# Kernel tuning notes

Measured on AMD Instinct MI355X. Metric: run time of the kernel, lower is better.

Reference implementation:

```python
import jax, jax.numpy as jnp
import numpy as np

GROUPS = 32
EPS = 1e-5


def group_norm(x, gamma, beta):
    # x: [B, C, H, W]; normalize over (C//G, H, W) within each of G groups
    B, C, H, W = x.shape
    xg = x.reshape(B, GROUPS, C // GROUPS, H, W)
    mean = xg.mean(axis=(2, 3, 4), keepdims=True)
    var = xg.var(axis=(2, 3, 4), keepdims=True)
    xg = (xg - mean) * jax.lax.rsqrt(var + EPS)
    x = xg.reshape(B, C, H, W)
    return x * gamma[None, :, None, None] + beta[None, :, None, None]


def conv1x1(x, W, b):
    # 1x1 conv == pointwise linear over channels. x: [B,C,H,W], W: [Cout,Cin]
    return jnp.einsum('oc,bchw->bohw', W, x) + b[None, :, None, None]


def setup_inputs() -> dict:
    key = jax.random.key(0)
    ks = jax.random.split(key, 6)
    B, C, H, W = 16, 512, 32, 32
    scale = 1.0 / np.sqrt(C)  # ~kaiming-ish init for 1x1 convs
    return {
        'x': jax.random.normal(ks[0], (B, C, H, W), jnp.float32),
        'gn_gamma': jnp.ones((C,), jnp.float32),
        'gn_beta': jnp.zeros((C,), jnp.float32),
        'Wq': jax.random.normal(ks[1], (C, C), jnp.float32) * scale,
        'bq': jnp.zeros((C,), jnp.float32),
        'Wk': jax.random.normal(ks[2], (C, C), jnp.float32) * scale,
        'bk': jnp.zeros((C,), jnp.float32),
        'Wv': jax.random.normal(ks[3], (C, C), jnp.float32) * scale,
        'bv': jnp.zeros((C,), jnp.float32),
        'Wp': jax.random.normal(ks[4], (C, C), jnp.float32) * scale,
        'bp': jnp.zeros((C,), jnp.float32),
    }


def reference(x, gn_gamma, gn_beta, Wq, bq, Wk, bk, Wv, bv, Wp, bp):
    B, C, H, W = x.shape
    h = group_norm(x, gn_gamma, gn_beta)
    q = conv1x1(h, Wq, bq).reshape(B, C, H * W)  # [B,C,T]
    k = conv1x1(h, Wk, bk).reshape(B, C, H * W)
    v = conv1x1(h, Wv, bv).reshape(B, C, H * W)
    # scores [B, T(query), S(key)] = q^T k, scaled by C^{-1/2}
    w = jnp.einsum('bct,bcs->bts', q, k) * (C ** -0.5)
    w = jax.nn.softmax(w, axis=-1)
    h = jnp.einsum('bts,bcs->bct', w, v).reshape(B, C, H, W)
    h = conv1x1(h, Wp, bp)
    return x + h
```

## Files before the change

kernel.cpp:

```cpp
#include <hip/hip_runtime.h>

typedef unsigned short u16;
typedef __bf16 bf16x8 __attribute__((ext_vector_type(8)));
typedef float f32x4 __attribute__((ext_vector_type(4)));
typedef float f32x16 __attribute__((ext_vector_type(16)));

__device__ __forceinline__ u16 f2bf(float f) {
    unsigned u = __builtin_bit_cast(unsigned, f);
    u += 0x7fffu + ((u >> 16) & 1u);
    return (u16)(u >> 16);
}
__device__ __forceinline__ float bf2f(u16 h) {
    return __builtin_bit_cast(float, (unsigned)h << 16);
}

#define GLDS16(g, l) __builtin_amdgcn_global_load_lds( \
    (const __attribute__((address_space(1))) void*)(g), \
    (__attribute__((address_space(3))) void*)(l), 16, 0, 0)

#define QK_SCALE 0.044194173824159216f

__global__ __launch_bounds__(256) void convert_kernel(
    const float* __restrict__ Wq, const float* __restrict__ Wk,
    const float* __restrict__ Wv, const float* __restrict__ Wp,
    const float* __restrict__ bq, const float* __restrict__ bk,
    const float* __restrict__ bv,
    u16* __restrict__ Wqkv, u16* __restrict__ Wpb, float* __restrict__ bqkv,
    float* __restrict__ rsum)
{
    int idx = blockIdx.x * 256 + threadIdx.x;
    if (idx < 786432) {
        int which = idx >> 18;
        int off   = idx & 262143;
        if (which == 0)
            Wqkv[idx] = f2bf(Wq[off] * QK_SCALE);
        else
            Wqkv[idx] = f2bf(((which == 1) ? Wk : Wv)[off]);
    } else {
        int off = idx - 786432;
        Wpb[off] = f2bf(Wp[off]);
    }
    if (idx < 1536) {
        float bvv = (idx < 512) ? bq[idx] * QK_SCALE
                  : (idx < 1024) ? bk[idx & 511] : bv[idx & 511];
        bqkv[idx] = bvv;
    }
    if (idx < 16384) rsum[idx] = 0.f;
}

__global__ __launch_bounds__(256) void gn_stats(
    const float* __restrict__ x, float2* __restrict__ stats)
{
    const int g = blockIdx.x, b = blockIdx.y, tid = threadIdx.x;
    const float* xg = x + ((size_t)b * 512 + (size_t)g * 16) * 1024;

    float s = 0.f, s2 = 0.f;
    const float4* x4 = (const float4*)xg;
    #pragma unroll 4
    for (int i = tid; i < 4096; i += 256) {
        float4 v = x4[i];
        s  += v.x + v.y + v.z + v.w;
        s2 += v.x * v.x + v.y * v.y + v.z * v.z + v.w * v.w;
    }
    #pragma unroll
    for (int off = 32; off; off >>= 1) {
        s  += __shfl_down(s, off);
        s2 += __shfl_down(s2, off);
    }
    __shared__ float rs[4], rs2[4];
    const int w = tid >> 6;
    if ((tid & 63) == 0) { rs[w] = s; rs2[w] = s2; }
    __syncthreads();
    if (tid == 0) {
        float S  = rs[0] + rs[1] + rs[2] + rs[3];
        float S2 = rs2[0] + rs2[1] + rs2[2] + rs2[3];
        float mean = S * (1.f / 16384.f);
        float var  = S2 * (1.f / 16384.f) - mean * mean;
        stats[b * 32 + g] = make_float2(mean, rsqrtf(var + 1e-5f));
    }
}

__global__ __launch_bounds__(256) void gn_apply(
    const float* __restrict__ x, const float* __restrict__ gamma,
    const float* __restrict__ beta, const float2* __restrict__ stats,
    u16* __restrict__ ht)
{
    const int tc = blockIdx.x, b = blockIdx.y, tid = threadIdx.x;
    const int t0 = tc * 32;

    __shared__ float2 st[32];
    __shared__ float ga[512], be[512];
    __shared__ __align__(16) u16 tile[512 * 32];

    if (tid < 32) st[tid] = stats[b * 32 + tid];
    for (int c = tid; c < 512; c += 256) { ga[c] = gamma[c]; be[c] = beta[c]; }
    __syncthreads();

    #pragma unroll
    for (int pass = 0; pass < 16; pass++) {
        const int c = pass * 32 + (tid >> 3);
        const int f = tid & 7;
        float4 v = *(const float4*)(x + ((size_t)(b * 512 + c)) * 1024 + t0 + f * 4);
        float2 s = st[c >> 4];
        float sc = s.y * ga[c];
        float sh = be[c] - s.x * sc;
        ushort4 hv = {f2bf(v.x * sc + sh), f2bf(v.y * sc + sh),
                      f2bf(v.z * sc + sh), f2bf(v.w * sc + sh)};
        const int slot = f ^ (c & 7) ^ ((c >> 3) & 7);
        *(ushort4*)(tile + c * 32 + slot * 4) = hv;
    }
    __syncthreads();

    #pragma unroll
    for (int p = 0; p < 8; p++) {
        const int t = p * 4 + (tid >> 6);
        const int l = tid & 63;
        u16 tmp[8];
        #pragma unroll
        for (int e = 0; e < 8; e++) {
            const int c = l * 8 + e;
            const int slot = (t >> 2) ^ (c & 7) ^ ((c >> 3) & 7);
            tmp[e] = tile[c * 32 + slot * 4 + (t & 3)];
        }
        *(uint4*)(ht + ((size_t)b * 1024 + t0 + t) * 512 + l * 8) = *(uint4*)tmp;
    }
}

template <int MODE>
__global__ __launch_bounds__(512, 2) void gemm_big(
    const u16* __restrict__ A, const u16* __restrict__ B,
    size_t strideA, size_t strideB, int lda, int ldb, int K,
    u16* __restrict__ o0, u16* __restrict__ o1, u16* __restrict__ o2,
    const float* __restrict__ bias)
{
    __shared__ __align__(16) u16 smem[73728];
    u16* As = smem;
    u16* Bs = smem + 49152;

    const int tid  = threadIdx.x;
    const int lane = tid & 63;
    const int wave = tid >> 6;
    const int wm   = (wave & 3) * 64;
    const int wn   = (wave >> 2) * 64;

    const int gx = gridDim.x, gy = gridDim.y;
    int f = blockIdx.x + gx * (blockIdx.y + gy * blockIdx.z);
    const int nwg = gx * gy * (int)gridDim.z;
    f = (f & 7) * (nwg >> 3) + (f >> 3);
    const int bx  = f % gx;
    const int byz = f / gx;
    const int by  = byz % gy;
    const int b   = byz / gy;

    const u16* Ab = A + (size_t)b * strideA + (size_t)by * 256 * lda;
    const u16* Bb = B + (size_t)b * strideB + (size_t)bx * 128 * ldb;

    const int srow = tid >> 3;
    const int sc   = tid & 7;
    const int scg  = sc ^ (srow & 7);

    const u16* aSrc[4]; int aDst[4];
    #pragma unroll
    for (int u = 0; u < 4; u++) {
        aSrc[u] = Ab + (size_t)(u * 64 + srow) * lda + scg * 8;
        aDst[u] = (u * 64 + srow) * 64 + sc * 8;
    }
    const u16* bSrc[2]; int bDst[2];
    #pragma unroll
    for (int u = 0; u < 2; u++) {
        bSrc[u] = Bb + (size_t)(u * 64 + srow) * ldb + scg * 8;
        bDst[u] = (u * 64 + srow) * 64 + sc * 8;
    }

    const int l15 = lane & 15, lh = lane >> 4, rx = lane & 7;
    int aOff[4][2], bOff[4][2];
    #pragma unroll
    for (int i = 0; i < 4; i++)
        #pragma unroll
        for (int ks = 0; ks < 2; ks++) {
            const int slot = ((ks << 2) + lh) ^ rx;
            aOff[i][ks] = (wm + i * 16 + l15) * 64 + slot * 8;
            bOff[i][ks] = (wn + i * 16 + l15) * 64 + slot * 8;
        }

    f32x4 acc[4][4] = {};
    const int NT = K >> 6;

    #pragma unroll
    for (int u = 0; u < 4; u++) GLDS16(aSrc[u], As + aDst[u]);
    #pragma unroll
    for (int u = 0; u < 2; u++) GLDS16(bSrc[u], Bs + bDst[u]);
    #pragma unroll
    for (int u = 0; u < 4; u++) GLDS16(aSrc[u] + 64, As + 16384 + aDst[u]);
    #pragma unroll
    for (int u = 0; u < 2; u++) GLDS16(bSrc[u] + 64, Bs + 8192 + bDst[u]);

    int cbuf = 0, sbuf = 2;
    for (int t = 0; t < NT; ++t) {
        if (t == NT - 1) asm volatile("s_waitcnt vmcnt(0)" ::: "memory");
        else             asm volatile("s_waitcnt vmcnt(6)" ::: "memory");
        __builtin_amdgcn_s_barrier();

        const u16* Ac = As + cbuf * 16384;
        const u16* Bc = Bs + cbuf * 8192;
        u16* Asb = As + sbuf * 16384;
        u16* Bsb = Bs + sbuf * 8192;
        const int ko = (t + 2) * 64;
        const bool pf = (t + 2 < NT);

        if (pf) {
            GLDS16(aSrc[0] + ko, Asb + aDst[0]);
            GLDS16(aSrc[1] + ko, Asb + aDst[1]);
            GLDS16(bSrc[0] + ko, Bsb + bDst[0]);
        }
        {
            bf16x8 af[4], bfr[4];
            #pragma unroll
            for (int i = 0; i < 4; i++) {
                af[i]  = *(const bf16x8*)(Ac + aOff[i][0]);
                bfr[i] = *(const bf16x8*)(Bc + bOff[i][0]);
            }
            __builtin_amdgcn_s_setprio(1);
            #pragma unroll
            for (int mi = 0; mi < 4; mi++)
                #pragma unroll
                for (int nj = 0; nj < 4; nj++)
                    acc[mi][nj] = __builtin_amdgcn_mfma_f32_16x16x32_bf16(
                        af[mi], bfr[nj], acc[mi][nj], 0, 0, 0);
            __builtin_amdgcn_s_setprio(0);
        }
        if (pf) {
            GLDS16(aSrc[2] + ko, Asb + aDst[2]);
            GLDS16(aSrc[3] + ko, Asb + aDst[3]);
            GLDS16(bSrc[1] + ko, Bsb + bDst[1]);
        }
        {
            bf16x8 af[4], bfr[4];
            #pragma unroll
            for (int i = 0; i < 4; i++) {
                af[i]  = *(const bf16x8*)(Ac + aOff[i][1]);
                bfr[i] = *(const bf16x8*)(Bc + bOff[i][1]);
            }
            __builtin_amdgcn_s_setprio(1);
            #pragma unroll
            for (int mi = 0; mi < 4; mi++)
                #pragma unroll
                for (int nj = 0; nj < 4; nj++)
                    acc[mi][nj] = __builtin_amdgcn_mfma_f32_16x16x32_bf16(
                        af[mi], bfr[nj], acc[mi][nj], 0, 0, 0);
            __builtin_amdgcn_s_setprio(0);
        }

        cbuf = (cbuf == 2) ? 0 : cbuf + 1;
        sbuf = (sbuf == 2) ? 0 : sbuf + 1;
    }

    const int N0 = bx * 128;
    const int M0 = by * 256;

    if (N0 < 1024) {
        u16* dst = (N0 < 512) ? o0 : o1;
        const int nn0 = N0 & 511;
        #pragma unroll
        for (int nj = 0; nj < 4; nj++) {
            const int n = wn + nj * 16 + l15;
            const float bv = bias[N0 + n];
            #pragma unroll
            for (int mi = 0; mi < 4; mi++) {
                const int mq = M0 + wm + mi * 16 + lh * 4;
                const size_t base = ((size_t)b * 1024 + mq) * 512 + nn0 + n;
                dst[base]        = f2bf(acc[mi][nj][0] + bv);
                dst[base + 512]  = f2bf(acc[mi][nj][1] + bv);
                dst[base + 1024] = f2bf(acc[mi][nj][2] + bv);
                dst[base + 1536] = f2bf(acc[mi][nj][3] + bv);
            }
        }
    } else {
        __syncthreads();
        #pragma unroll
        for (int mi = 0; mi < 4; mi++) {
            const int mq = wm + mi * 16 + lh * 4;
            #pragma unroll
            for (int nj = 0; nj < 4; nj++) {
                const int n = wn + nj * 16 + l15;
                const float bv = bias[N0 + n];
                ushort4 hv = {f2bf(acc[mi][nj][0] + bv), f2bf(acc[mi][nj][1] + bv),
                              f2bf(acc[mi][nj][2] + bv), f2bf(acc[mi][nj][3] + bv)};
                *(ushort4*)((char*)smem + n * 512 +
                            (((mq >> 3) ^ (n & 31)) << 4) + ((mq >> 2) & 1) * 8) = hv;
            }
        }
        __syncthreads();
        #pragma unroll
        for (int p = 0; p < 8; p++) {
            const int n  = p * 16 + (tid >> 5);
            const int gi = tid & 31;
            uint4 v4 = *(const uint4*)((char*)smem + n * 512 +
                                       ((gi ^ (n & 31)) << 4));
            u16* dst = o2 + ((size_t)b * 512 + (N0 - 1024) + n) * 1024 + M0;
            *(uint4*)(dst + gi * 8) = v4;
        }
    }
}

template <int MODE>
__global__ __launch_bounds__(256, 4) void gemm128(
    const u16* __restrict__ A, const u16* __restrict__ B,
    size_t strideA, size_t strideB, int lda, int ldb, int K,
    u16* __restrict__ o0,
    float* __restrict__ fo, const float* __restrict__ bias,
    const float* __restrict__ xres)
{
    __shared__ __align__(16) u16 sm[16384];
    u16* As = sm;
    u16* Bs = sm + 8192;

    const int tid   = threadIdx.x;
    const int lane  = tid & 63;
    const int wave  = tid >> 6;
    const int wm    = (wave >> 1) * 64;
    const int wn    = (wave & 1) * 64;
    const int l31   = lane & 31;
    const int khalf = lane >> 5;

    const int gx = gridDim.x, gy = gridDim.y;
    int f = blockIdx.x + gx * (blockIdx.y + gy * blockIdx.z);
    const int nwg = gx * gy * (int)gridDim.z;
    f = (f & 7) * (nwg >> 3) + (f >> 3);
    const int bx  = f % gx;
    const int byz = f / gx;
    const int by  = byz % gy;
    const int b   = byz / gy;

    const u16* Ab = A + (size_t)b * strideA + (size_t)by * 128 * lda;
    const u16* Bb = B + (size_t)b * strideB + (size_t)bx * 128 * ldb;

    const int srow = lane >> 3;
    const int sc   = lane & 7;
    const int scg  = sc ^ srow;

    f32x16 acc[2][2] = {};

    for (int k0 = 0; k0 < K; k0 += 64) {
        __syncthreads();
        #pragma unroll
        for (int s = 0; s < 4; s++) {
            const int r = wave * 32 + s * 8 + srow;
            GLDS16(Ab + (size_t)r * lda + k0 + scg * 8, As + r * 64 + sc * 8);
            GLDS16(Bb + (size_t)r * ldb + k0 + scg * 8, Bs + r * 64 + sc * 8);
        }
        __syncthreads();

        #pragma unroll
        for (int ks = 0; ks < 4; ks++) {
            const int cidx = ks * 2 + khalf;
            const int slot = (cidx ^ (lane & 7)) * 8;
            bf16x8 af[2], bfr[2];
            #pragma unroll
            for (int i = 0; i < 2; i++)
                af[i] = *(const bf16x8*)(As + (wm + i * 32 + l31) * 64 + slot);
            #pragma unroll
            for (int j = 0; j < 2; j++)
                bfr[j] = *(const bf16x8*)(Bs + (wn + j * 32 + l31) * 64 + slot);
            #pragma unroll
            for (int i = 0; i < 2; i++)
                #pragma unroll
                for (int j = 0; j < 2; j++)
                    acc[i][j] = __builtin_amdgcn_mfma_f32_32x32x16_bf16(
                        af[i], bfr[j], acc[i][j], 0, 0, 0);
        }
    }

    const int N0 = bx * 128;
    const int M0 = by * 128;

    if (MODE != 3) {
        __syncthreads();
        float rinv_[2];
        if (MODE == 2) {
            #pragma unroll
            for (int j = 0; j < 2; j++)
                rinv_[j] = 1.0f / xres[(size_t)b * 1024 + N0 + wn + j * 32 + l31];
        }
        #pragma unroll
        for (int i = 0; i < 2; i++) {
            #pragma unroll
            for (int j = 0; j < 2; j++) {
                const int n = wn + j * 32 + l31;
                #pragma unroll
                for (int g = 0; g < 4; g++) {
                    const int m = wm + 4 * khalf + i * 32 + 8 * g;
                    float a0 = acc[i][j][4 * g],     a1 = acc[i][j][4 * g + 1];
                    float a2 = acc[i][j][4 * g + 2], a3 = acc[i][j][4 * g + 3];
                    if (MODE == 1) {
                        a0 = __expf(a0); a1 = __expf(a1);
                        a2 = __expf(a2); a3 = __expf(a3);
                    }
                    if (MODE == 2) {
                        a0 *= rinv_[j]; a1 *= rinv_[j];
                        a2 *= rinv_[j]; a3 *= rinv_[j];
                    }
                    ushort4 hv = {f2bf(a0), f2bf(a1), f2bf(a2), f2bf(a3)};
                    *(ushort4*)(sm + n * 128 + (((m >> 3) ^ (n & 15)) << 3) + (m & 7)) = hv;
                }
            }
        }
        __syncthreads();
        #pragma unroll
        for (int p = 0; p < 8; p++) {
            const int n  = p * 16 + (tid >> 4);
            const int gi = tid & 15;
            uint4 v = *(const uint4*)(sm + n * 128 + ((gi ^ (n & 15)) << 3));
            u16* dst;
            if (MODE == 1) dst = o0 + ((size_t)b * 1024 + N0 + n) * 1024 + M0;
            else           dst = o0 + ((size_t)b * 1024 + N0 + n) * 512 + M0;
            *(uint4*)(dst + gi * 8) = v;
            if (MODE == 1) {
                unsigned wd_[4] = {v.x, v.y, v.z, v.w};
                float rsm = 0.f;
                #pragma unroll
                for (int q = 0; q < 4; q++)
                    rsm += __builtin_bit_cast(float, wd_[q] << 16)
                         + __builtin_bit_cast(float, wd_[q] & 0xffff0000u);
                #pragma unroll
                for (int off = 1; off < 16; off <<= 1)
                    rsm += __shfl_xor(rsm, off);
                if (gi == 0)
                    atomicAdd(fo + ((size_t)b * 1024 + N0 + n), rsm);
            }
        }
    } else {
        float* smf = (float*)sm;
        #pragma unroll
        for (int i = 0; i < 2; i++) {
            __syncthreads();
            #pragma unroll
            for (int j = 0; j < 2; j++) {
                const int n = wn + j * 32 + l31;
                #pragma unroll
                for (int g = 0; g < 4; g++) {
                    const int mIdx = 4 * khalf + 8 * g + ((wm >> 6) << 5);
                    float4 v4 = {acc[i][j][4 * g],     acc[i][j][4 * g + 1],
                                 acc[i][j][4 * g + 2], acc[i][j][4 * g + 3]};
                    *(float4*)(smf + n * 64 + (((mIdx >> 2) ^ (n & 15)) << 2)) = v4;
                }
            }
            __syncthreads();
            #pragma unroll
            for (int p = 0; p < 8; p++) {
                const int n  = p * 16 + (tid >> 4);
                const int gi = tid & 15;
                float4 v = *(const float4*)(smf + n * 64 + ((gi ^ (n & 15)) << 2));
                const int m = (gi & 7) * 4 + ((gi >> 3) << 6) + 32 * i;
                const size_t off = ((size_t)b * 512 + N0 + n) * 1024 + M0 + m;
                const float bv = bias[N0 + n];
                const float4 xv = *(const float4*)(xres + off);
                float4 ov = {v.x + bv + xv.x, v.y + bv + xv.y,
                             v.z + bv + xv.z, v.w + bv + xv.w};
                *(float4*)(fo + off) = ov;
            }
        }
    }
}

extern "C" void kernel_launch(void* const* d_in, const int* in_sizes, int n_in,
                              void* d_out, int out_size, void* d_ws, size_t ws_size,
                              hipStream_t stream)
{
    const float* x     = (const float*)d_in[0];
    const float* gamma = (const float*)d_in[1];
    const float* beta  = (const float*)d_in[2];
    const float* Wq    = (const float*)d_in[3];
    const float* bq    = (const float*)d_in[4];
    const float* Wk    = (const float*)d_in[5];
    const float* bk    = (const float*)d_in[6];
    const float* Wv    = (const float*)d_in[7];
    const float* bv    = (const float*)d_in[8];
    const float* Wp    = (const float*)d_in[9];
    const float* bp    = (const float*)d_in[10];

    char* ws = (char*)d_ws;
    u16*   Wqkv   = (u16*)(ws + 0);
    u16*   Wpb    = (u16*)(ws + 1572864);
    float* bqkv   = (float*)(ws + 2097152);
    u16*   ht     = (u16*)(ws + 2105344);
    u16*   kt     = (u16*)(ws + 18882560);
    u16*   vv     = (u16*)(ws + 35659776);
    u16*   scores = (u16*)(ws + 52436992);
    u16*   qt  = (u16*)d_out;
    float2* stats = (float2*)((char*)d_out + 16777216);
    float* rsum   = (float*)((char*)d_out + 16781312);
    u16*   h2  = ht;
    float* out = (float*)d_out;

    convert_kernel<<<4096, 256, 0, stream>>>(Wq, Wk, Wv, Wp, bq, bk, bv,
                                             Wqkv, Wpb, bqkv, rsum);
    gn_stats<<<dim3(32, 16), 256, 0, stream>>>(x, stats);
    gn_apply<<<dim3(32, 16), 256, 0, stream>>>(x, gamma, beta, stats, ht);

    gemm_big<0><<<dim3(12, 4, 16), 512, 0, stream>>>(
        ht, Wqkv, 524288, 0, 512, 512, 512,
        qt, kt, vv, bqkv);

    gemm128<1><<<dim3(8, 8, 16), 256, 0, stream>>>(
        kt, qt, 524288, 524288, 512, 512, 512,
        scores, rsum, nullptr, nullptr);

    gemm128<2><<<dim3(8, 4, 16), 256, 0, stream>>>(
        vv, scores, 524288, 1048576, 1024, 1024, 1024,
        h2, nullptr, nullptr, rsum);

    gemm128<3><<<dim3(4, 8, 16), 256, 0, stream>>>(
        h2, Wpb, 524288, 0, 512, 512, 512,
        nullptr, out, bp, x);
}
```

Before: 227.1 us.

## Switch gemm128 to 16x16x32 MFMA tiles and fuse weight conversion with GN stats

```diff
diff --git a/kernel.cpp b/kernel.cpp
--- a/kernel.cpp
+++ b/kernel.cpp
@@ -3,7 +3,6 @@
 typedef unsigned short u16;
 typedef __bf16 bf16x8 __attribute__((ext_vector_type(8)));
 typedef float f32x4 __attribute__((ext_vector_type(4)));
-typedef float f32x16 __attribute__((ext_vector_type(16)));
 
 __device__ __forceinline__ u16 f2bf(float f) {
     unsigned u = __builtin_bit_cast(unsigned, f);
@@ -20,38 +19,42 @@
 
 #define QK_SCALE 0.044194173824159216f
 
-__global__ __launch_bounds__(256) void convert_kernel(
+__global__ __launch_bounds__(256) void fused_pre(
     const float* __restrict__ Wq, const float* __restrict__ Wk,
     const float* __restrict__ Wv, const float* __restrict__ Wp,
     const float* __restrict__ bq, const float* __restrict__ bk,
     const float* __restrict__ bv,
     u16* __restrict__ Wqkv, u16* __restrict__ Wpb, float* __restrict__ bqkv,
-    float* __restrict__ rsum)
-{
-    int idx = blockIdx.x * 256 + threadIdx.x;
-    if (idx < 786432) {
-        int which = idx >> 18;
-        int off   = idx & 262143;
-        if (which == 0)
-            Wqkv[idx] = f2bf(Wq[off] * QK_SCALE);
-        else
-            Wqkv[idx] = f2bf(((which == 1) ? Wk : Wv)[off]);
-    } else {
-        int off = idx - 786432;
-        Wpb[off] = f2bf(Wp[off]);
-    }
-    if (idx < 1536) {
-        float bvv = (idx < 512) ? bq[idx] * QK_SCALE
-                  : (idx < 1024) ? bk[idx & 511] : bv[idx & 511];
-        bqkv[idx] = bvv;
-    }
-    if (idx < 16384) rsum[idx] = 0.f;
-}
-
-__global__ __launch_bounds__(256) void gn_stats(
+    float* __restrict__ rsum,
     const float* __restrict__ x, float2* __restrict__ stats)
 {
-    const int g = blockIdx.x, b = blockIdx.y, tid = threadIdx.x;
+    __shared__ float rs[4], rs2[4];
+    const int tid = threadIdx.x;
+
+    if (blockIdx.x < 4096) {
+        int idx = blockIdx.x * 256 + tid;
+        if (idx < 786432) {
+            int which = idx >> 18;
+            int off   = idx & 262143;
+            if (which == 0)
+                Wqkv[idx] = f2bf(Wq[off] * QK_SCALE);
+            else
+                Wqkv[idx] = f2bf(((which == 1) ? Wk : Wv)[off]);
+        } else {
+            int off = idx - 786432;
+            Wpb[off] = f2bf(Wp[off]);
+        }
+        if (idx < 1536) {
+            float bvv = (idx < 512) ? bq[idx] * QK_SCALE
+                      : (idx < 1024) ? bk[idx & 511] : bv[idx & 511];
+            bqkv[idx] = bvv;
+        }
+        if (idx < 16384) rsum[idx] = 0.f;
+        return;
+    }
+
+    const int rem = blockIdx.x - 4096;
+    const int g = rem & 31, b = rem >> 5;
     const float* xg = x + ((size_t)b * 512 + (size_t)g * 16) * 1024;
 
     float s = 0.f, s2 = 0.f;
@@ -67,7 +70,6 @@
         s  += __shfl_down(s, off);
         s2 += __shfl_down(s2, off);
     }
-    __shared__ float rs[4], rs2[4];
     const int w = tid >> 6;
     if ((tid & 63) == 0) { rs[w] = s; rs2[w] = s2; }
     __syncthreads();
@@ -315,13 +317,14 @@
     u16* As = sm;
     u16* Bs = sm + 8192;
 
-    const int tid   = threadIdx.x;
-    const int lane  = tid & 63;
-    const int wave  = tid >> 6;
-    const int wm    = (wave >> 1) * 64;
-    const int wn    = (wave & 1) * 64;
-    const int l31   = lane & 31;
-    const int khalf = lane >> 5;
+    const int tid  = threadIdx.x;
+    const int lane = tid & 63;
+    const int wave = tid >> 6;
+    const int wm   = (wave >> 1) * 64;
+    const int wn   = (wave & 1) * 64;
+    const int l15  = lane & 15;
+    const int lh   = lane >> 4;
+    const int rx   = lane & 7;
 
     const int gx = gridDim.x, gy = gridDim.y;
     int f = blockIdx.x + gx * (blockIdx.y + gy * blockIdx.z);
@@ -339,7 +342,17 @@
     const int sc   = lane & 7;
     const int scg  = sc ^ srow;
 
-    f32x16 acc[2][2] = {};
+    int aOff[4][2], bOff[4][2];
+    #pragma unroll
+    for (int i = 0; i < 4; i++)
+        #pragma unroll
+        for (int ks = 0; ks < 2; ks++) {
+            const int slot = ((ks << 2) + lh) ^ rx;
+            aOff[i][ks] = (wm + i * 16 + l15) * 64 + slot * 8;
+            bOff[i][ks] = (wn + i * 16 + l15) * 64 + slot * 8;
+        }
+
+    f32x4 acc[4][4] = {};
 
     for (int k0 = 0; k0 < K; k0 += 64) {
         __syncthreads();
@@ -352,22 +365,21 @@
         __syncthreads();
 
         #pragma unroll
-        for (int ks = 0; ks < 4; ks++) {
-            const int cidx = ks * 2 + khalf;
-            const int slot = (cidx ^ (lane & 7)) * 8;
-            bf16x8 af[2], bfr[2];
-            #pragma unroll
-            for (int i = 0; i < 2; i++)
-                af[i] = *(const bf16x8*)(As + (wm + i * 32 + l31) * 64 + slot);
-            #pragma unroll
-            for (int j = 0; j < 2; j++)
-                bfr[j] = *(const bf16x8*)(Bs + (wn + j * 32 + l31) * 64 + slot);
-            #pragma unroll
-            for (int i = 0; i < 2; i++)
+        for (int ks = 0; ks < 2; ks++) {
+            bf16x8 af[4], bfr[4];
+            #pragma unroll
+            for (int i = 0; i < 4; i++) {
+                af[i]  = *(const bf16x8*)(As + aOff[i][ks]);
+                bfr[i] = *(const bf16x8*)(Bs + bOff[i][ks]);
+            }
+            __builtin_amdgcn_s_setprio(1);
+            #pragma unroll
+            for (int mi = 0; mi < 4; mi++)
                 #pragma unroll
-                for (int j = 0; j < 2; j++)
-                    acc[i][j] = __builtin_amdgcn_mfma_f32_32x32x16_bf16(
-                        af[i], bfr[j], acc[i][j], 0, 0, 0);
+                for (int nj = 0; nj < 4; nj++)
+                    acc[mi][nj] = __builtin_amdgcn_mfma_f32_16x16x32_bf16(
+                        af[mi], bfr[nj], acc[mi][nj], 0, 0, 0);
+            __builtin_amdgcn_s_setprio(0);
         }
     }
 
@@ -376,33 +388,33 @@
 
     if (MODE != 3) {
         __syncthreads();
-        float rinv_[2];
+        float rinv_[4];
         if (MODE == 2) {
             #pragma unroll
-            for (int j = 0; j < 2; j++)
-                rinv_[j] = 1.0f / xres[(size_t)b * 1024 + N0 + wn + j * 32 + l31];
-        }
-        #pragma unroll
-        for (int i = 0; i < 2; i++) {
-            #pragma unroll
-            for (int j = 0; j < 2; j++) {
-                const int n = wn + j * 32 + l31;
-                #pragma unroll
-                for (int g = 0; g < 4; g++) {
-                    const int m = wm + 4 * khalf + i * 32 + 8 * g;
-                    float a0 = acc[i][j][4 * g],     a1 = acc[i][j][4 * g + 1];
-                    float a2 = acc[i][j][4 * g + 2], a3 = acc[i][j][4 * g + 3];
-                    if (MODE == 1) {
-                        a0 = __expf(a0); a1 = __expf(a1);
-                        a2 = __expf(a2); a3 = __expf(a3);
-                    }
-                    if (MODE == 2) {
-                        a0 *= rinv_[j]; a1 *= rinv_[j];
-                        a2 *= rinv_[j]; a3 *= rinv_[j];
-                    }
-                    ushort4 hv = {f2bf(a0), f2bf(a1), f2bf(a2), f2bf(a3)};
-                    *(ushort4*)(sm + n * 128 + (((m >> 3) ^ (n & 15)) << 3) + (m & 7)) = hv;
+            for (int nj = 0; nj < 4; nj++)
+                rinv_[nj] = 1.0f / xres[(size_t)b * 1024 + N0 + wn + nj * 16 + l15];
+        }
+        #pragma unroll
+        for (int mi = 0; mi < 4; mi++) {
+            const int mq  = wm + mi * 16 + lh * 4;
+            const int gsl = mq >> 3;
+            const int gb  = ((mq >> 2) & 1) * 8;
+            #pragma unroll
+            for (int nj = 0; nj < 4; nj++) {
+                const int n = wn + nj * 16 + l15;
+                float a0 = acc[mi][nj][0], a1 = acc[mi][nj][1];
+                float a2 = acc[mi][nj][2], a3 = acc[mi][nj][3];
+                if (MODE == 1) {
+                    a0 = __expf(a0); a1 = __expf(a1);
+                    a2 = __expf(a2); a3 = __expf(a3);
                 }
+                if (MODE == 2) {
+                    a0 *= rinv_[nj]; a1 *= rinv_[nj];
+                    a2 *= rinv_[nj]; a3 *= rinv_[nj];
+                }
+                ushort4 hv = {f2bf(a0), f2bf(a1), f2bf(a2), f2bf(a3)};
+                *(ushort4*)((char*)sm + n * 256 +
+                            ((gsl ^ (n & 15)) << 4) + gb) = hv;
             }
         }
         __syncthreads();
@@ -410,7 +422,7 @@
         for (int p = 0; p < 8; p++) {
             const int n  = p * 16 + (tid >> 4);
             const int gi = tid & 15;
-            uint4 v = *(const uint4*)(sm + n * 128 + ((gi ^ (n & 15)) << 3));
+            uint4 v = *(const uint4*)((char*)sm + n * 256 + ((gi ^ (n & 15)) << 4));
             u16* dst;
             if (MODE == 1) dst = o0 + ((size_t)b * 1024 + N0 + n) * 1024 + M0;
             else           dst = o0 + ((size_t)b * 1024 + N0 + n) * 512 + M0;
@@ -432,17 +444,21 @@
     } else {
         float* smf = (float*)sm;
         #pragma unroll
-        for (int i = 0; i < 2; i++) {
+        for (int half = 0; half < 2; half++) {
             __syncthreads();
-            #pragma unroll
-            for (int j = 0; j < 2; j++) {
-                const int n = wn + j * 32 + l31;
+            if ((wave >> 1) == half) {
                 #pragma unroll
-                for (int g = 0; g < 4; g++) {
-                    const int mIdx = 4 * khalf + 8 * g + ((wm >> 6) << 5);
-                    float4 v4 = {acc[i][j][4 * g],     acc[i][j][4 * g + 1],
-                                 acc[i][j][4 * g + 2], acc[i][j][4 * g + 3]};
-                    *(float4*)(smf + n * 64 + (((mIdx >> 2) ^ (n & 15)) << 2)) = v4;
+                for (int mi = 0; mi < 4; mi++) {
+                    const int mloc = mi * 16 + lh * 4;
+                    const int gsl  = mloc >> 2;
+                    #pragma unroll
+                    for (int nj = 0; nj < 4; nj++) {
+                        const int n = wn + nj * 16 + l15;
+                        float4 v4 = {acc[mi][nj][0], acc[mi][nj][1],
+                                     acc[mi][nj][2], acc[mi][nj][3]};
+                        *(float4*)((char*)smf + n * 256 +
+                                   ((gsl ^ (n & 15)) << 4)) = v4;
+                    }
                 }
             }
             __syncthreads();
@@ -450,8 +466,9 @@
             for (int p = 0; p < 8; p++) {
                 const int n  = p * 16 + (tid >> 4);
                 const int gi = tid & 15;
-                float4 v = *(const float4*)(smf + n * 64 + ((gi ^ (n & 15)) << 2));
-                const int m = (gi & 7) * 4 + ((gi >> 3) << 6) + 32 * i;
+                float4 v = *(const float4*)((char*)smf + n * 256 +
+                                            ((gi ^ (n & 15)) << 4));
+                const int m = half * 64 + gi * 4;
                 const size_t off = ((size_t)b * 512 + N0 + n) * 1024 + M0 + m;
                 const float bv = bias[N0 + n];
                 const float4 xv = *(const float4*)(xres + off);
@@ -493,9 +510,8 @@
     u16*   h2  = ht;
     float* out = (float*)d_out;
 
-    convert_kernel<<<4096, 256, 0, stream>>>(Wq, Wk, Wv, Wp, bq, bk, bv,
-                                             Wqkv, Wpb, bqkv, rsum);
-    gn_stats<<<dim3(32, 16), 256, 0, stream>>>(x, stats);
+    fused_pre<<<4608, 256, 0, stream>>>(Wq, Wk, Wv, Wp, bq, bk, bv,
+                                        Wqkv, Wpb, bqkv, rsum, x, stats);
     gn_apply<<<dim3(32, 16), 256, 0, stream>>>(x, gamma, beta, stats, ht);
 
     gemm_big<0><<<dim3(12, 4, 16), 512, 0, stream>>>(
```

Result: faster. 221.4 us (-2.5%).
